# Kernel tuning notes

Measured on AMD Instinct MI355X. Metric: run time of the kernel, lower is better.

The kernel has to match this reference:

```python
import jax, jax.numpy as jnp
import numpy as np

N_NODES = 10000
EPS = 1e-5


def _layernorm(x, gamma, beta):
    mu = jnp.mean(x, axis=-1, keepdims=True)
    var = jnp.mean(jnp.square(x - mu), axis=-1, keepdims=True)
    return (x - mu) * jax.lax.rsqrt(var + EPS) * gamma + beta


def _sage_pool_layer(h, src, dst, Wp, bp, Ws, Wn, b, gamma, beta):
    # DGL SAGEConv(aggregator='pool'):
    #   m_u = relu(h_u @ Wp^T + bp); h_neigh[v] = max_{u in N(v)} m_u (0 if no neighbors)
    #   rst = h @ Ws^T + h_neigh @ Wn^T + b
    m = jax.nn.relu(h @ Wp.T + bp)              # [N, d]
    msg = m[src]                                 # [E, d] gather
    agg = jax.ops.segment_max(msg, dst, num_segments=N_NODES)
    agg = jnp.where(jnp.isfinite(agg), agg, 0.0)  # isolated nodes -> 0
    rst = h @ Ws.T + agg @ Wn.T + b
    # gsage_layer: LayerNorm, then Encoder applies relu (dropout inactive in eval)
    return jax.nn.relu(_layernorm(rst, gamma, beta))


def setup_inputs() -> dict:
    key = jax.random.key(0)
    ks = jax.random.split(key, 16)
    d = 256
    E = 320000
    s = 1.0 / np.sqrt(d)
    inp = {
        "h": jax.random.normal(ks[0], (N_NODES, d), dtype=jnp.float32),
        "edge_src": jax.random.randint(ks[1], (E,), 0, N_NODES, dtype=jnp.int32),
        "edge_dst": jax.random.randint(ks[2], (E,), 0, N_NODES, dtype=jnp.int32),
    }
    for li in range(2):
        kk = jax.random.split(ks[3 + li], 3)
        inp[f"Wp{li}"] = jax.random.normal(kk[0], (d, d), dtype=jnp.float32) * s
        inp[f"bp{li}"] = jnp.zeros((d,), jnp.float32)
        inp[f"Ws{li}"] = jax.random.normal(kk[1], (d, d), dtype=jnp.float32) * s
        inp[f"Wn{li}"] = jax.random.normal(kk[2], (d, d), dtype=jnp.float32) * s
        inp[f"b{li}"] = jnp.zeros((d,), jnp.float32)
        inp[f"g{li}"] = jnp.ones((d,), jnp.float32)
        inp[f"be{li}"] = jnp.zeros((d,), jnp.float32)
    return inp


def reference(h, edge_src, edge_dst,
              Wp0, bp0, Ws0, Wn0, b0, g0, be0,
              Wp1, bp1, Ws1, Wn1, b1, g1, be1):
    h = _sage_pool_layer(h, edge_src, edge_dst, Wp0, bp0, Ws0, Wn0, b0, g0, be0)
    h = _sage_pool_layer(h, edge_src, edge_dst, Wp1, bp1, Ws1, Wn1, b1, g1, be1)
    return h
```

## Files before the change

kernel.cpp:

```cpp
#include <hip/hip_runtime.h>

#define D 256
#define CAP 128
#define ASTRIDE 280
#define LN_EPS 1e-5f

typedef short short8 __attribute__((ext_vector_type(8)));
typedef float floatx4 __attribute__((ext_vector_type(4)));
typedef unsigned short u16x4 __attribute__((ext_vector_type(4)));

typedef const __attribute__((address_space(1))) void* gas_t;
typedef __attribute__((address_space(3))) void* las_t;

#define WAIT_VM(n) __builtin_amdgcn_s_waitcnt(((n) & 0xF) | (((n) >> 4) << 14) | (7 << 4) | (0xF << 8))

__device__ __forceinline__ u16x4 umax4(u16x4 a, u16x4 b) {
#if __has_builtin(__builtin_elementwise_max)
    return __builtin_elementwise_max(a, b);
#else
    u16x4 r;
    r.x = a.x > b.x ? a.x : b.x; r.y = a.y > b.y ? a.y : b.y;
    r.z = a.z > b.z ? a.z : b.z; r.w = a.w > b.w ? a.w : b.w;
    return r;
#endif
}

__device__ __forceinline__ unsigned short f2b(float f) {
    union { float f; unsigned int u; } x; x.f = f;
    unsigned int u = x.u + 0x7FFFu + ((x.u >> 16) & 1u);
    return (unsigned short)(u >> 16);
}

__device__ __forceinline__ short8 ldA_f32(const float* p) {
    const float4 a = *(const float4*)p;
    const float4 b = *(const float4*)(p + 4);
    short8 r;
    r[0] = (short)f2b(a.x); r[1] = (short)f2b(a.y);
    r[2] = (short)f2b(a.z); r[3] = (short)f2b(a.w);
    r[4] = (short)f2b(b.x); r[5] = (short)f2b(b.y);
    r[6] = (short)f2b(b.z); r[7] = (short)f2b(b.w);
    return r;
}

#define GEMM_HALF(A_EXPR, WPTR, K0H)                                            \
    {                                                                           \
        short8 aF[4], bF[4][4];                                                 \
        _Pragma("unroll") for (int ks = 0; ks < 4; ks++)                        \
            aF[ks] = A_EXPR(K0H + ks * 32);                                     \
        _Pragma("unroll") for (int ks = 0; ks < 4; ks++)                        \
        _Pragma("unroll") for (int t = 0; t < 4; t++)                           \
            bF[ks][t] = *(const short8*)((WPTR) + t * 16 * D + (K0H) + ks * 32);\
        _Pragma("unroll") for (int ks = 0; ks < 4; ks++) {                      \
            acc[0] = __builtin_amdgcn_mfma_f32_16x16x32_bf16(aF[ks], bF[ks][0], acc[0], 0, 0, 0); \
            acc[1] = __builtin_amdgcn_mfma_f32_16x16x32_bf16(aF[ks], bF[ks][1], acc[1], 0, 0, 0); \
            acc[2] = __builtin_amdgcn_mfma_f32_16x16x32_bf16(aF[ks], bF[ks][2], acc[2], 0, 0, 0); \
            acc[3] = __builtin_amdgcn_mfma_f32_16x16x32_bf16(aF[ks], bF[ks][3], acc[3], 0, 0, 0); \
        }                                                                       \
    }

__global__ __launch_bounds__(256) void prep_kernel(
    const float* __restrict__ w0, const float* __restrict__ w1,
    const float* __restrict__ w2, const float* __restrict__ w3,
    const float* __restrict__ w4, const float* __restrict__ w5,
    unsigned short* __restrict__ wb,
    int* __restrict__ cnt, unsigned short* __restrict__ mb, int N)
{
    const int blk = blockIdx.x;
    const int tid = threadIdx.x;
    if (blk < 384) {
        const int wsel = blk >> 6;
        const float* src;
        switch (wsel) {
            case 0: src = w0; break; case 1: src = w1; break;
            case 2: src = w2; break; case 3: src = w3; break;
            case 4: src = w4; break; default: src = w5; break;
        }
        const int idx = (blk & 63) * 1024 + tid * 4;
        const float4 v = *(const float4*)(src + idx);
        ushort4 o;
        o.x = f2b(v.x); o.y = f2b(v.y); o.z = f2b(v.z); o.w = f2b(v.w);
        *(ushort4*)(wb + (size_t)wsel * 65536 + idx) = o;
    } else if (blk < 424) {
        const int i = (blk - 384) * 256 + tid;
        if (i < N) cnt[i] = 0;
    } else {
        mb[(size_t)N * D + tid] = 0;
    }
}

__global__ __launch_bounds__(64, 4) void gemm_relu(
    const float* __restrict__ Af, const unsigned short* __restrict__ Ab,
    const unsigned short* __restrict__ W,
    const float* __restrict__ bias, unsigned short* __restrict__ out_b, int nrow,
    const int* __restrict__ esrc, const int* __restrict__ edst,
    int* __restrict__ cnt, unsigned short* __restrict__ csr, int E, int ngemm)
{
    if ((int)blockIdx.x >= ngemm) {
        const int nsb = gridDim.x - ngemm;
        int i = ((int)blockIdx.x - ngemm) * 64 + threadIdx.x;
        const int stride = nsb * 64;
        for (; i < E; i += stride) {
            const int d = edst[i];
            const int pos = atomicAdd(&cnt[d], 1);
            if (pos < CAP) csr[(size_t)d * CAP + pos] = (unsigned short)esrc[i];
        }
        return;
    }

    const int blk = blockIdx.x;
    const int g = blk >> 5;
    const int o = blk & 31;
    const int c = o >> 3;
    const int r = g * 8 + (o & 7);
    if (r >= nrow) return;

    const int lane = threadIdx.x;
    const int quad = lane >> 4;
    const int l16 = lane & 15;
    const int row0 = r * 16;
    const int col0 = c * 64;
    const int koff = quad * 8;

    floatx4 acc[4];
#pragma unroll
    for (int t = 0; t < 4; t++) acc[t] = (floatx4)(0.f);

    const unsigned short* aptr = Ab ? Ab + (size_t)(row0 + l16) * D + koff : nullptr;
    const float*          afp  = Af ? Af + (size_t)(row0 + l16) * D + koff : nullptr;
    const unsigned short* wptr = W + (size_t)(col0 + l16) * D + koff;
#define A_SRC(K) (Af ? ldA_f32(afp + (K)) : *(const short8*)(aptr + (K)))
    GEMM_HALF(A_SRC, wptr, 0)
    GEMM_HALF(A_SRC, wptr, 128)
#undef A_SRC

#pragma unroll
    for (int t = 0; t < 4; t++) {
        const float bcol = bias[col0 + t * 16 + l16];
#pragma unroll
        for (int rr = 0; rr < 4; rr++) {
            const int rg = row0 + quad * 4 + rr;
            const int col = col0 + t * 16 + l16;
            out_b[(size_t)rg * D + col] = f2b(fmaxf(acc[t][rr] + bcol, 0.f));
        }
    }
}

__global__ __launch_bounds__(256, 3) void gemm_ln_pool(
    const float* __restrict__ Af, const unsigned short* __restrict__ Ab,
    const unsigned short* __restrict__ Wself,
    const unsigned short* __restrict__ Wneigh,
    const unsigned short* __restrict__ mpool,
    const int* __restrict__ cnt, const unsigned short* __restrict__ csr,
    const float* __restrict__ bias,
    const float* __restrict__ gamma, const float* __restrict__ beta,
    unsigned short* __restrict__ out_b, float* __restrict__ out_f, int N)
{
    __shared__ unsigned short idxS[16][CAP];
    __shared__ unsigned short gbuf[4][2][8][D];
    __shared__ unsigned short aggS[16 * ASTRIDE];
    __shared__ float redS[4][16], redS2[4][16], muA[16], rsA[16];

    const int tid = threadIdx.x;
    const int wave = tid >> 6;
    const int lane = tid & 63;
    const int quad = lane >> 4;
    const int l16 = lane & 15;
    const int row0 = blockIdx.x * 16;
    const int koff = quad * 8;
    const int rbase = wave * 4;
    const int half = lane >> 5;
    const int l32 = lane & 31;

    int degs[4];
#pragma unroll
    for (int rr = 0; rr < 4; rr++) degs[rr] = min(cnt[row0 + rbase + rr], CAP);
    int P = max(max(degs[0], degs[1]), max(degs[2], degs[3]));
    const int P2 = (P + 1) & ~1;
#pragma unroll
    for (int rr = 0; rr < 4; rr++) {
        const int rg = row0 + rbase + rr;
        for (int i = lane; i < P2; i += 64)
            idxS[rbase + rr][i] = (i < degs[rr]) ? csr[(size_t)rg * CAP + i]
                                                 : (unsigned short)N;
    }

    floatx4 acc[4];
#pragma unroll
    for (int t = 0; t < 4; t++) acc[t] = (floatx4)(0.f);

    {
        const unsigned short* aptr = Ab ? Ab + (size_t)(row0 + l16) * D + koff : nullptr;
        const float*          afp  = Af ? Af + (size_t)(row0 + l16) * D + koff : nullptr;
        const unsigned short* wptr = Wself + (size_t)(wave * 64 + l16) * D + koff;
#pragma unroll
        for (int k0 = 0; k0 < D; k0 += 32) {
            const short8 av = Af ? ldA_f32(afp + k0) : *(const short8*)(aptr + k0);
            const short8 b0 = *(const short8*)(wptr + k0);
            const short8 b1 = *(const short8*)(wptr + 16 * D + k0);
            const short8 b2 = *(const short8*)(wptr + 32 * D + k0);
            const short8 b3 = *(const short8*)(wptr + 48 * D + k0);
            acc[0] = __builtin_amdgcn_mfma_f32_16x16x32_bf16(av, b0, acc[0], 0, 0, 0);
            acc[1] = __builtin_amdgcn_mfma_f32_16x16x32_bf16(av, b1, acc[1], 0, 0, 0);
            acc[2] = __builtin_amdgcn_mfma_f32_16x16x32_bf16(av, b2, acc[2], 0, 0, 0);
            acc[3] = __builtin_amdgcn_mfma_f32_16x16x32_bf16(av, b3, acc[3], 0, 0, 0);
        }
    }

    {
        const int nb = P2 >> 1;
        u16x4 mx[4];
#pragma unroll
        for (int rr = 0; rr < 4; rr++) mx[rr] = (u16x4)(0);

#define ISSUE_BURST(bi, buf)                                                    \
        {                                                                       \
            _Pragma("unroll") for (int rr = 0; rr < 4; rr++) {                  \
                const int jj = idxS[rbase + rr][2 * (bi) + half];               \
                const unsigned short* gp = mpool + (size_t)jj * D + l32 * 8;    \
                __builtin_amdgcn_global_load_lds(                               \
                    (gas_t)gp, (las_t)&gbuf[wave][buf][rr * 2][0], 16, 0, 0);   \
            }                                                                   \
        }

        if (nb > 0) ISSUE_BURST(0, 0);
        if (nb > 1) ISSUE_BURST(1, 1);
        for (int b = 0; b < nb; b++) {
            if (b + 1 < nb) WAIT_VM(4); else WAIT_VM(0);
            const int buf = b & 1;
#pragma unroll
            for (int rr = 0; rr < 4; rr++) {
                const u16x4 a0 = *(const u16x4*)&gbuf[wave][buf][rr * 2 + 0][lane * 4];
                const u16x4 a1 = *(const u16x4*)&gbuf[wave][buf][rr * 2 + 1][lane * 4];
                mx[rr] = umax4(mx[rr], umax4(a0, a1));
            }
            if (b + 2 < nb) ISSUE_BURST(b + 2, buf);
        }
#undef ISSUE_BURST
#pragma unroll
        for (int rr = 0; rr < 4; rr++)
            *(u16x4*)&aggS[(rbase + rr) * ASTRIDE + lane * 4] = mx[rr];
    }
    __syncthreads();

    {
        const unsigned short* wptr = Wneigh + (size_t)(wave * 64 + l16) * D + koff;
#pragma unroll
        for (int k0 = 0; k0 < D; k0 += 32) {
            const short8 av = *(const short8*)&aggS[l16 * ASTRIDE + koff + k0];
            const short8 b0 = *(const short8*)(wptr + k0);
            const short8 b1 = *(const short8*)(wptr + 16 * D + k0);
            const short8 b2 = *(const short8*)(wptr + 32 * D + k0);
            const short8 b3 = *(const short8*)(wptr + 48 * D + k0);
            acc[0] = __builtin_amdgcn_mfma_f32_16x16x32_bf16(av, b0, acc[0], 0, 0, 0);
            acc[1] = __builtin_amdgcn_mfma_f32_16x16x32_bf16(av, b1, acc[1], 0, 0, 0);
            acc[2] = __builtin_amdgcn_mfma_f32_16x16x32_bf16(av, b2, acc[2], 0, 0, 0);
            acc[3] = __builtin_amdgcn_mfma_f32_16x16x32_bf16(av, b3, acc[3], 0, 0, 0);
        }
    }

    float bcol[4];
#pragma unroll
    for (int t = 0; t < 4; t++) bcol[t] = bias[wave * 64 + t * 16 + l16];
#pragma unroll
    for (int t = 0; t < 4; t++)
#pragma unroll
        for (int r = 0; r < 4; r++) acc[t][r] += bcol[t];

#pragma unroll
    for (int r = 0; r < 4; r++) {
        float s = 0.f, s2 = 0.f;
#pragma unroll
        for (int t = 0; t < 4; t++) {
            const float v = acc[t][r];
            s += v; s2 += v * v;
        }
        s += __shfl_xor(s, 1);  s2 += __shfl_xor(s2, 1);
        s += __shfl_xor(s, 2);  s2 += __shfl_xor(s2, 2);
        s += __shfl_xor(s, 4);  s2 += __shfl_xor(s2, 4);
        s += __shfl_xor(s, 8);  s2 += __shfl_xor(s2, 8);
        if (l16 == 0) {
            redS[wave][quad * 4 + r] = s;
            redS2[wave][quad * 4 + r] = s2;
        }
    }
    __syncthreads();
    if (tid < 16) {
        const float S  = redS[0][tid] + redS[1][tid] + redS[2][tid] + redS[3][tid];
        const float S2 = redS2[0][tid] + redS2[1][tid] + redS2[2][tid] + redS2[3][tid];
        const float mu = S * (1.f / D);
        float var = S2 * (1.f / D) - mu * mu;
        var = fmaxf(var, 0.f);
        muA[tid] = mu;
        rsA[tid] = rsqrtf(var + LN_EPS);
    }
    __syncthreads();

    float gcol[4], becol[4];
#pragma unroll
    for (int t = 0; t < 4; t++) {
        gcol[t] = gamma[wave * 64 + t * 16 + l16];
        becol[t] = beta[wave * 64 + t * 16 + l16];
    }
#pragma unroll
    for (int r = 0; r < 4; r++) {
        const int rl = quad * 4 + r;
        const int rg = row0 + rl;
        const float mu = muA[rl];
        const float rs = rsA[rl];
#pragma unroll
        for (int t = 0; t < 4; t++) {
            const int col = wave * 64 + t * 16 + l16;
            float o = (acc[t][r] - mu) * rs * gcol[t] + becol[t];
            o = fmaxf(o, 0.f);
            if (out_f) out_f[(size_t)rg * D + col] = o;
            else       out_b[(size_t)rg * D + col] = f2b(o);
        }
    }
}

extern "C" void kernel_launch(void* const* d_in, const int* in_sizes, int n_in,
                              void* d_out, int out_size, void* d_ws, size_t ws_size,
                              hipStream_t stream) {
    const float* h    = (const float*)d_in[0];
    const int*   esrc = (const int*)d_in[1];
    const int*   edst = (const int*)d_in[2];
    const float* Wp0  = (const float*)d_in[3];
    const float* bp0  = (const float*)d_in[4];
    const float* Ws0  = (const float*)d_in[5];
    const float* Wn0  = (const float*)d_in[6];
    const float* b0   = (const float*)d_in[7];
    const float* g0   = (const float*)d_in[8];
    const float* be0  = (const float*)d_in[9];
    const float* Wp1  = (const float*)d_in[10];
    const float* bp1  = (const float*)d_in[11];
    const float* Ws1  = (const float*)d_in[12];
    const float* Wn1  = (const float*)d_in[13];
    const float* b1   = (const float*)d_in[14];
    const float* g1   = (const float*)d_in[15];
    const float* be1  = (const float*)d_in[16];

    const int N = in_sizes[0] / D;
    const int E = in_sizes[1];
    const size_t ND = (size_t)N * D;

    unsigned short* mb  = (unsigned short*)d_ws;
    unsigned short* h1b = mb + ND + D;
    unsigned short* wb  = h1b + ND;
    int* cnt = (int*)(wb + 6 * 65536);
    unsigned short* csr = (unsigned short*)(cnt + N);

    unsigned short* wpb0 = wb + 0 * 65536;
    unsigned short* wsb0 = wb + 1 * 65536;
    unsigned short* wnb0 = wb + 2 * 65536;
    unsigned short* wpb1 = wb + 3 * 65536;
    unsigned short* wsb1 = wb + 4 * 65536;
    unsigned short* wnb1 = wb + 5 * 65536;

    const int nrow = N / 16;
    const int rblocks = ((nrow + 7) / 8) * 32;
    const int pblocks = nrow;
    const int sblocks = 1024;

    prep_kernel<<<425, 256, 0, stream>>>(Wp0, Ws0, Wn0, Wp1, Ws1, Wn1, wb,
                                         cnt, mb, N);

    gemm_relu<<<rblocks + sblocks, 64, 0, stream>>>(h, nullptr, wpb0, bp0, mb, nrow,
                                                    esrc, edst, cnt, csr, E, rblocks);
    gemm_ln_pool<<<pblocks, 256, 0, stream>>>(h, nullptr, wsb0, wnb0, mb, cnt, csr,
                                              b0, g0, be0, h1b, nullptr, N);

    gemm_relu<<<rblocks, 64, 0, stream>>>(nullptr, h1b, wpb1, bp1, mb, nrow,
                                          esrc, edst, cnt, csr, 0, rblocks);
    gemm_ln_pool<<<pblocks, 256, 0, stream>>>(nullptr, h1b, wsb1, wnb1, mb, cnt, csr,
                                              b1, g1, be1, nullptr, (float*)d_out, N);
}
```

Measured before the change: 217.5 us.

## Specialize waves in pool kernel: two GEMM waves, four gather-max waves

The fused self-GEMM/neighbor-max/LayerNorm kernel now uses 6 waves per block. Waves 2-5 only do the neighbor gather and max-pool into shared memory. Waves 0-1 do the self GEMM at the same time, each over 128 output columns with 8 accumulators, then the neighbor GEMM and LayerNorm. This overlaps the latency-bound gather with MFMA work instead of running them back to back in every wave, but it doubles accumulator registers in the GEMM waves and leaves four waves idle after the barrier.

```diff
diff --git a/kernel.cpp b/kernel.cpp
--- a/kernel.cpp
+++ b/kernel.cpp
@@ -145,7 +145,7 @@
     }
 }
 
-__global__ __launch_bounds__(256, 3) void gemm_ln_pool(
+__global__ __launch_bounds__(384, 4) void gemm_ln_pool(
     const float* __restrict__ Af, const unsigned short* __restrict__ Ab,
     const unsigned short* __restrict__ Wself,
     const unsigned short* __restrict__ Wneigh,
@@ -158,7 +158,7 @@
     __shared__ unsigned short idxS[16][CAP];
     __shared__ unsigned short gbuf[4][2][8][D];
     __shared__ unsigned short aggS[16 * ASTRIDE];
-    __shared__ float redS[4][16], redS2[4][16], muA[16], rsA[16];
+    __shared__ float redS[2][16], redS2[2][16], muA[16], rsA[16];
 
     const int tid = threadIdx.x;
     const int wave = tid >> 6;
@@ -167,46 +167,30 @@
     const int l16 = lane & 15;
     const int row0 = blockIdx.x * 16;
     const int koff = quad * 8;
-    const int rbase = wave * 4;
-    const int half = lane >> 5;
-    const int l32 = lane & 31;
-
-    int degs[4];
-#pragma unroll
-    for (int rr = 0; rr < 4; rr++) degs[rr] = min(cnt[row0 + rbase + rr], CAP);
-    int P = max(max(degs[0], degs[1]), max(degs[2], degs[3]));
-    const int P2 = (P + 1) & ~1;
-#pragma unroll
-    for (int rr = 0; rr < 4; rr++) {
-        const int rg = row0 + rbase + rr;
-        for (int i = lane; i < P2; i += 64)
-            idxS[rbase + rr][i] = (i < degs[rr]) ? csr[(size_t)rg * CAP + i]
-                                                 : (unsigned short)N;
-    }
-
-    floatx4 acc[4];
-#pragma unroll
-    for (int t = 0; t < 4; t++) acc[t] = (floatx4)(0.f);
-
-    {
-        const unsigned short* aptr = Ab ? Ab + (size_t)(row0 + l16) * D + koff : nullptr;
-        const float*          afp  = Af ? Af + (size_t)(row0 + l16) * D + koff : nullptr;
-        const unsigned short* wptr = Wself + (size_t)(wave * 64 + l16) * D + koff;
-#pragma unroll
-        for (int k0 = 0; k0 < D; k0 += 32) {
-            const short8 av = Af ? ldA_f32(afp + k0) : *(const short8*)(aptr + k0);
-            const short8 b0 = *(const short8*)(wptr + k0);
-            const short8 b1 = *(const short8*)(wptr + 16 * D + k0);
-            const short8 b2 = *(const short8*)(wptr + 32 * D + k0);
-            const short8 b3 = *(const short8*)(wptr + 48 * D + k0);
-            acc[0] = __builtin_amdgcn_mfma_f32_16x16x32_bf16(av, b0, acc[0], 0, 0, 0);
-            acc[1] = __builtin_amdgcn_mfma_f32_16x16x32_bf16(av, b1, acc[1], 0, 0, 0);
-            acc[2] = __builtin_amdgcn_mfma_f32_16x16x32_bf16(av, b2, acc[2], 0, 0, 0);
-            acc[3] = __builtin_amdgcn_mfma_f32_16x16x32_bf16(av, b3, acc[3], 0, 0, 0);
-        }
-    }
-
-    {
+
+    floatx4 acc[8];
+#pragma unroll
+    for (int t = 0; t < 8; t++) acc[t] = (floatx4)(0.f);
+
+    if (wave >= 2) {
+        const int pw = wave - 2;
+        const int rbase = pw * 4;
+        const int half = lane >> 5;
+        const int l32 = lane & 31;
+
+        int degs[4];
+#pragma unroll
+        for (int rr = 0; rr < 4; rr++) degs[rr] = min(cnt[row0 + rbase + rr], CAP);
+        int P = max(max(degs[0], degs[1]), max(degs[2], degs[3]));
+        const int P2 = (P + 1) & ~1;
+#pragma unroll
+        for (int rr = 0; rr < 4; rr++) {
+            const int rg = row0 + rbase + rr;
+            for (int i = lane; i < P2; i += 64)
+                idxS[rbase + rr][i] = (i < degs[rr]) ? csr[(size_t)rg * CAP + i]
+                                                     : (unsigned short)N;
+        }
+
         const int nb = P2 >> 1;
         u16x4 mx[4];
 #pragma unroll
@@ -218,7 +202,7 @@
                 const int jj = idxS[rbase + rr][2 * (bi) + half];               \
                 const unsigned short* gp = mpool + (size_t)jj * D + l32 * 8;    \
                 __builtin_amdgcn_global_load_lds(                               \
-                    (gas_t)gp, (las_t)&gbuf[wave][buf][rr * 2][0], 16, 0, 0);   \
+                    (gas_t)gp, (las_t)&gbuf[pw][buf][rr * 2][0], 16, 0, 0);     \
             }                                                                   \
         }
 
@@ -229,8 +213,8 @@
             const int buf = b & 1;
 #pragma unroll
             for (int rr = 0; rr < 4; rr++) {
-                const u16x4 a0 = *(const u16x4*)&gbuf[wave][buf][rr * 2 + 0][lane * 4];
-                const u16x4 a1 = *(const u16x4*)&gbuf[wave][buf][rr * 2 + 1][lane * 4];
+                const u16x4 a0 = *(const u16x4*)&gbuf[pw][buf][rr * 2 + 0][lane * 4];
+                const u16x4 a1 = *(const u16x4*)&gbuf[pw][buf][rr * 2 + 1][lane * 4];
                 mx[rr] = umax4(mx[rr], umax4(a0, a1));
             }
             if (b + 2 < nb) ISSUE_BURST(b + 2, buf);
@@ -239,54 +223,66 @@
 #pragma unroll
         for (int rr = 0; rr < 4; rr++)
             *(u16x4*)&aggS[(rbase + rr) * ASTRIDE + lane * 4] = mx[rr];
+    } else {
+        const unsigned short* aptr = Ab ? Ab + (size_t)(row0 + l16) * D + koff : nullptr;
+        const float*          afp  = Af ? Af + (size_t)(row0 + l16) * D + koff : nullptr;
+        const unsigned short* wptr = Wself + (size_t)(wave * 128 + l16) * D + koff;
+#pragma unroll
+        for (int k0 = 0; k0 < D; k0 += 32) {
+            const short8 av = Af ? ldA_f32(afp + k0) : *(const short8*)(aptr + k0);
+            short8 bv[8];
+#pragma unroll
+            for (int t = 0; t < 8; t++)
+                bv[t] = *(const short8*)(wptr + t * 16 * D + k0);
+#pragma unroll
+            for (int t = 0; t < 8; t++)
+                acc[t] = __builtin_amdgcn_mfma_f32_16x16x32_bf16(av, bv[t], acc[t], 0, 0, 0);
+        }
     }
     __syncthreads();
 
-    {
-        const unsigned short* wptr = Wneigh + (size_t)(wave * 64 + l16) * D + koff;
+    if (wave < 2) {
+        const unsigned short* wptr = Wneigh + (size_t)(wave * 128 + l16) * D + koff;
 #pragma unroll
         for (int k0 = 0; k0 < D; k0 += 32) {
             const short8 av = *(const short8*)&aggS[l16 * ASTRIDE + koff + k0];
-            const short8 b0 = *(const short8*)(wptr + k0);
-            const short8 b1 = *(const short8*)(wptr + 16 * D + k0);
-            const short8 b2 = *(const short8*)(wptr + 32 * D + k0);
-            const short8 b3 = *(const short8*)(wptr + 48 * D + k0);
-            acc[0] = __builtin_amdgcn_mfma_f32_16x16x32_bf16(av, b0, acc[0], 0, 0, 0);
-            acc[1] = __builtin_amdgcn_mfma_f32_16x16x32_bf16(av, b1, acc[1], 0, 0, 0);
-            acc[2] = __builtin_amdgcn_mfma_f32_16x16x32_bf16(av, b2, acc[2], 0, 0, 0);
-            acc[3] = __builtin_amdgcn_mfma_f32_16x16x32_bf16(av, b3, acc[3], 0, 0, 0);
-        }
-    }
-
-    float bcol[4];
-#pragma unroll
-    for (int t = 0; t < 4; t++) bcol[t] = bias[wave * 64 + t * 16 + l16];
-#pragma unroll
-    for (int t = 0; t < 4; t++)
-#pragma unroll
-        for (int r = 0; r < 4; r++) acc[t][r] += bcol[t];
-
-#pragma unroll
-    for (int r = 0; r < 4; r++) {
-        float s = 0.f, s2 = 0.f;
-#pragma unroll
-        for (int t = 0; t < 4; t++) {
-            const float v = acc[t][r];
-            s += v; s2 += v * v;
-        }
-        s += __shfl_xor(s, 1);  s2 += __shfl_xor(s2, 1);
-        s += __shfl_xor(s, 2);  s2 += __shfl_xor(s2, 2);
-        s += __shfl_xor(s, 4);  s2 += __shfl_xor(s2, 4);
-        s += __shfl_xor(s, 8);  s2 += __shfl_xor(s2, 8);
-        if (l16 == 0) {
-            redS[wave][quad * 4 + r] = s;
-            redS2[wave][quad * 4 + r] = s2;
+            short8 bv[8];
+#pragma unroll
+            for (int t = 0; t < 8; t++)
+                bv[t] = *(const short8*)(wptr + t * 16 * D + k0);
+#pragma unroll
+            for (int t = 0; t < 8; t++)
+                acc[t] = __builtin_amdgcn_mfma_f32_16x16x32_bf16(av, bv[t], acc[t], 0, 0, 0);
+        }
+
+#pragma unroll
+        for (int t = 0; t < 8; t++) {
+            const float bcol = bias[wave * 128 + t * 16 + l16];
+#pragma unroll
+            for (int r = 0; r < 4; r++) acc[t][r] += bcol;
+        }
+#pragma unroll
+        for (int r = 0; r < 4; r++) {
+            float s = 0.f, s2 = 0.f;
+#pragma unroll
+            for (int t = 0; t < 8; t++) {
+                const float v = acc[t][r];
+                s += v; s2 += v * v;
+            }
+            s += __shfl_xor(s, 1);  s2 += __shfl_xor(s2, 1);
+            s += __shfl_xor(s, 2);  s2 += __shfl_xor(s2, 2);
+            s += __shfl_xor(s, 4);  s2 += __shfl_xor(s2, 4);
+            s += __shfl_xor(s, 8);  s2 += __shfl_xor(s2, 8);
+            if (l16 == 0) {
+                redS[wave][quad * 4 + r] = s;
+                redS2[wave][quad * 4 + r] = s2;
+            }
         }
     }
     __syncthreads();
     if (tid < 16) {
-        const float S  = redS[0][tid] + redS[1][tid] + redS[2][tid] + redS[3][tid];
-        const float S2 = redS2[0][tid] + redS2[1][tid] + redS2[2][tid] + redS2[3][tid];
+        const float S  = redS[0][tid] + redS[1][tid];
+        const float S2 = redS2[0][tid] + redS2[1][tid];
         const float mu = S * (1.f / D);
         float var = S2 * (1.f / D) - mu * mu;
         var = fmaxf(var, 0.f);
@@ -295,25 +291,21 @@
     }
     __syncthreads();
 
-    float gcol[4], becol[4];
-#pragma unroll
-    for (int t = 0; t < 4; t++) {
-        gcol[t] = gamma[wave * 64 + t * 16 + l16];
-        becol[t] = beta[wave * 64 + t * 16 + l16];
-    }
-#pragma unroll
-    for (int r = 0; r < 4; r++) {
-        const int rl = quad * 4 + r;
-        const int rg = row0 + rl;
-        const float mu = muA[rl];
-        const float rs = rsA[rl];
-#pragma unroll
-        for (int t = 0; t < 4; t++) {
-            const int col = wave * 64 + t * 16 + l16;
-            float o = (acc[t][r] - mu) * rs * gcol[t] + becol[t];
-            o = fmaxf(o, 0.f);
-            if (out_f) out_f[(size_t)rg * D + col] = o;
-            else       out_b[(size_t)rg * D + col] = f2b(o);
+    if (wave < 2) {
+#pragma unroll
+        for (int r = 0; r < 4; r++) {
+            const int rl = quad * 4 + r;
+            const int rg = row0 + rl;
+            const float mu = muA[rl];
+            const float rs = rsA[rl];
+#pragma unroll
+            for (int t = 0; t < 8; t++) {
+                const int col = wave * 128 + t * 16 + l16;
+                float o = (acc[t][r] - mu) * rs * gamma[col] + beta[col];
+                o = fmaxf(o, 0.f);
+                if (out_f) out_f[(size_t)rg * D + col] = o;
+                else       out_b[(size_t)rg * D + col] = f2b(o);
+            }
         }
     }
 }
@@ -366,11 +358,11 @@
 
     gemm_relu<<<rblocks + sblocks, 64, 0, stream>>>(h, nullptr, wpb0, bp0, mb, nrow,
                                                     esrc, edst, cnt, csr, E, rblocks);
-    gemm_ln_pool<<<pblocks, 256, 0, stream>>>(h, nullptr, wsb0, wnb0, mb, cnt, csr,
+    gemm_ln_pool<<<pblocks, 384, 0, stream>>>(h, nullptr, wsb0, wnb0, mb, cnt, csr,
                                               b0, g0, be0, h1b, nullptr, N);
 
     gemm_relu<<<rblocks, 64, 0, stream>>>(nullptr, h1b, wpb1, bp1, mb, nrow,
                                           esrc, edst, cnt, csr, 0, rblocks);
-    gemm_ln_pool<<<pblocks, 256, 0, stream>>>(nullptr, h1b, wsb1, wnb1, mb, cnt, csr,
+    gemm_ln_pool<<<pblocks, 384, 0, stream>>>(nullptr, h1b, wsb1, wnb1, mb, cnt, csr,
                                               b1, g1, be1, nullptr, (float*)d_out, N);
 }
```

Result: slower. 221.9 us (+2.0%).
